# Performance work log

Measured on AMD Instinct MI355X. Metric: run time of the kernel, lower is better.

Reference implementation:

```python
import jax, jax.numpy as jnp
import numpy as np

B, D, N, C = 8192, 128, 64, 256

def setup_inputs() -> dict:
    key = jax.random.key(0)
    ks = jax.random.split(key, 7)
    s1 = 1.0 / np.sqrt(D)
    s2 = 1.0 / np.sqrt(C)
    return {
        "X": jax.random.normal(ks[0], (B, D, N), dtype=jnp.float32),
        "W1": jax.random.normal(ks[1], (D, C), dtype=jnp.float32) * s1,
        "b1": jax.random.normal(ks[2], (C,), dtype=jnp.float32) * s1,
        "W2": jax.random.normal(ks[3], (C, C), dtype=jnp.float32) * s2,
        "b2": jax.random.normal(ks[4], (C,), dtype=jnp.float32) * s2,
        "W3": jax.random.normal(ks[5], (C, 1), dtype=jnp.float32) * s2,
        "b3": jax.random.normal(ks[6], (1,), dtype=jnp.float32) * s2,
    }

def reference(X, W1, b1, W2, b2, W3, b3):
    # X: (B, D, N); each per-node slice X[:, :, i] goes through the shared MLP.
    # Batched over nodes: one GEMM instead of N tiny launches.
    h = jax.nn.relu(jnp.einsum('bdn,dc->bnc', X, W1) + b1)   # (B, N, C)
    h = jax.nn.relu(jnp.einsum('bnc,ce->bne', h, W2) + b2)   # (B, N, C)
    logits = jnp.einsum('bnc,co->bno', h, W3) + b3           # (B, N, 1)
    logits = logits[..., 0]                                   # (B, N)
    zeros = jnp.zeros((X.shape[0], 1), dtype=logits.dtype)    # add_zero=True
    return jnp.concatenate([zeros, logits], axis=1)           # (B, N+1)
```

## Files before the change

### kernel.cpp

```cpp
#include <hip/hip_runtime.h>
#include <hip/hip_bf16.h>

typedef unsigned short u16;
typedef unsigned int   u32;
typedef __attribute__((ext_vector_type(8))) short bf16x8;
typedef __attribute__((ext_vector_type(4))) float f32x4;

#define NB 8192

__device__ __forceinline__ u32 pack2bf(float a, float b) {
    __hip_bfloat162 h = __float22bfloat162_rn(make_float2(a, b));
    return *reinterpret_cast<u32*>(&h);
}

__device__ __forceinline__ u16 f2bf(float x) {
    u32 u = __float_as_uint(x);
    u32 r = u + 0x7FFFu + ((u >> 16) & 1u);
    return (u16)(r >> 16);
}

__global__ __launch_bounds__(256) void prep_weights(
    const float* __restrict__ W1, const float* __restrict__ W2,
    u16* __restrict__ w1fr, u16* __restrict__ w2fr)
{
    int tid = blockIdx.x * 256 + threadIdx.x;
    if (tid < 32768) {
        const int f = tid >> 9, r = tid & 511, l = r >> 3, j = r & 7;
        const int wv = f >> 4, mt = (f >> 2) & 3, ks = f & 3;
        const int c = 64 * wv + 16 * mt + (l & 15);
        const int d = 32 * ks + 8 * (l >> 4) + j;
        w1fr[tid] = f2bf(W1[d * 256 + c]);
    } else {
        const int t2 = tid - 32768;
        if (t2 < 65536) {
            const int f = t2 >> 9, r = t2 & 511, l = r >> 3, j = r & 7;
            const int wv = f >> 5, et = (f >> 3) & 3, ks = f & 7;
            const int e = 64 * wv + 16 * et + (l & 15);
            const int c = 32 * ks + 8 * (l >> 4) + j;
            w2fr[t2] = f2bf(W2[c * 256 + e]);
        }
    }
}

__global__ __launch_bounds__(256, 4) void fused_mlp(
    const float* __restrict__ X,
    const float* __restrict__ b1, const float* __restrict__ b2,
    const float* __restrict__ W3, const float* __restrict__ b3,
    const u16* __restrict__ w1fr, const u16* __restrict__ w2fr,
    float* __restrict__ out)
{
    __shared__ u16 smem[64 * 256];
    u16* xt   = smem;
    u16* h1s  = smem;
    float* partl = (float*)smem;

    const int tid = threadIdx.x;
    const int w   = tid >> 6;
    const int l   = tid & 63;
    const int lc  = l & 15;
    const int lk  = l >> 4;
    const int b   = blockIdx.x;
    const float* Xb = X + (size_t)b * 8192;

    const u16* w1b = w1fr + w * 8192  + l * 8;
    const u16* w2b = w2fr + w * 16384 + l * 8;

    #pragma unroll
    for (int it = 0; it < 4; ++it) {
        const int dc = w + 4 * it, d0 = dc << 3;
        float v[8];
        #pragma unroll
        for (int j = 0; j < 8; ++j) v[j] = Xb[(d0 + j) * 64 + l];
        u32 pk[4];
        #pragma unroll
        for (int j = 0; j < 4; ++j) pk[j] = pack2bf(v[2 * j], v[2 * j + 1]);
        *(uint4*)(xt + l * 128 + ((dc ^ lc) << 3)) = make_uint4(pk[0], pk[1], pk[2], pk[3]);
    }

    bf16x8 afrN[4];
    #pragma unroll
    for (int mt = 0; mt < 4; ++mt)
        afrN[mt] = *(const bf16x8*)(w1b + mt * 2048);
    __syncthreads();

    f32x4 acc[4][4];
    #pragma unroll
    for (int mt = 0; mt < 4; ++mt)
        #pragma unroll
        for (int nt = 0; nt < 4; ++nt) acc[mt][nt] = (f32x4){0.f, 0.f, 0.f, 0.f};

    #pragma unroll
    for (int ks = 0; ks < 4; ++ks) {
        bf16x8 afr[4], bfr[4];
        #pragma unroll
        for (int mt = 0; mt < 4; ++mt) afr[mt] = afrN[mt];
        if (ks < 3) {
            #pragma unroll
            for (int mt = 0; mt < 4; ++mt)
                afrN[mt] = *(const bf16x8*)(w1b + (mt * 4 + ks + 1) * 512);
        }
        #pragma unroll
        for (int nt = 0; nt < 4; ++nt)
            bfr[nt] = *(const bf16x8*)(xt + (16 * nt + lc) * 128 + (((4 * ks + lk) ^ lc) << 3));
        #pragma unroll
        for (int mt = 0; mt < 4; ++mt)
            #pragma unroll
            for (int nt = 0; nt < 4; ++nt)
                acc[mt][nt] = __builtin_amdgcn_mfma_f32_16x16x32_bf16(afr[mt], bfr[nt], acc[mt][nt], 0, 0, 0);
    }
    __syncthreads();

    #pragma unroll
    for (int mt = 0; mt < 4; ++mt) {
        const int c0 = 64 * w + 16 * mt + 4 * lk;
        const float4 bv = *(const float4*)(b1 + c0);
        #pragma unroll
        for (int nt = 0; nt < 4; ++nt) {
            const int n = 16 * nt + lc;
            float x0 = fmaxf(acc[mt][nt][0] + bv.x, 0.f);
            float x1 = fmaxf(acc[mt][nt][1] + bv.y, 0.f);
            float x2 = fmaxf(acc[mt][nt][2] + bv.z, 0.f);
            float x3 = fmaxf(acc[mt][nt][3] + bv.w, 0.f);
            const int chunk = (c0 >> 3) ^ lc;
            *(uint2*)(h1s + n * 256 + (chunk << 3) + (c0 & 7)) =
                make_uint2(pack2bf(x0, x1), pack2bf(x2, x3));
        }
    }

    bf16x8 bfrN[4];
    #pragma unroll
    for (int nt = 0; nt < 4; ++nt)
        bfrN[nt] = *(const bf16x8*)(w2b + nt * 4096);
    __syncthreads();

    f32x4 acc2[4][4];
    #pragma unroll
    for (int mt = 0; mt < 4; ++mt)
        #pragma unroll
        for (int nt = 0; nt < 4; ++nt) acc2[mt][nt] = (f32x4){0.f, 0.f, 0.f, 0.f};

    #pragma unroll
    for (int ks = 0; ks < 8; ++ks) {
        bf16x8 afr[4], bfr[4];
        #pragma unroll
        for (int nt = 0; nt < 4; ++nt) bfr[nt] = bfrN[nt];
        if (ks < 7) {
            #pragma unroll
            for (int nt = 0; nt < 4; ++nt)
                bfrN[nt] = *(const bf16x8*)(w2b + (nt * 8 + ks + 1) * 512);
        }
        #pragma unroll
        for (int mt = 0; mt < 4; ++mt)
            afr[mt] = *(const bf16x8*)(h1s + (16 * mt + lc) * 256 + (((4 * ks + lk) ^ lc) << 3));
        #pragma unroll
        for (int mt = 0; mt < 4; ++mt)
            #pragma unroll
            for (int nt = 0; nt < 4; ++nt)
                acc2[mt][nt] = __builtin_amdgcn_mfma_f32_16x16x32_bf16(afr[mt], bfr[nt], acc2[mt][nt], 0, 0, 0);
    }
    __syncthreads();

    float b2v[4], w3v[4];
    #pragma unroll
    for (int nt = 0; nt < 4; ++nt) {
        const int e = 64 * w + 16 * nt + lc;
        b2v[nt] = b2[e];
        w3v[nt] = W3[e];
    }
    #pragma unroll
    for (int mt = 0; mt < 4; ++mt) {
        #pragma unroll
        for (int j = 0; j < 4; ++j) {
            float s = 0.f;
            #pragma unroll
            for (int nt = 0; nt < 4; ++nt)
                s += fmaxf(acc2[mt][nt][j] + b2v[nt], 0.f) * w3v[nt];
            s += __shfl_xor(s, 1);
            s += __shfl_xor(s, 2);
            s += __shfl_xor(s, 4);
            s += __shfl_xor(s, 8);
            if (lc == 0) partl[w * 64 + 16 * mt + 4 * lk + j] = s;
        }
    }
    __syncthreads();

    if (tid < 64) {
        float s = partl[0 * 64 + tid] + partl[1 * 64 + tid] + partl[2 * 64 + tid] + partl[3 * 64 + tid] + b3[0];
        out[(size_t)b * 65 + 1 + tid] = s;
    } else if (tid == 64) {
        out[(size_t)b * 65] = 0.f;
    }
}

extern "C" void kernel_launch(void* const* d_in, const int* in_sizes, int n_in,
                              void* d_out, int out_size, void* d_ws, size_t ws_size,
                              hipStream_t stream) {
    const float* X  = (const float*)d_in[0];
    const float* W1 = (const float*)d_in[1];
    const float* b1 = (const float*)d_in[2];
    const float* W2 = (const float*)d_in[3];
    const float* b2 = (const float*)d_in[4];
    const float* W3 = (const float*)d_in[5];
    const float* b3 = (const float*)d_in[6];
    float* out = (float*)d_out;

    u16* w1fr = (u16*)d_ws;
    u16* w2fr = w1fr + 32768;

    prep_weights<<<384, 256, 0, stream>>>(W1, W2, w1fr, w2fr);
    fused_mlp<<<NB, 256, 0, stream>>>(X, b1, b2, W3, b3, w1fr, w2fr, out);
}
```

Baseline: 122.2 us.

## Split fused MLP across eight waves per block with separate LDS buffers

Doubles the block to 512 threads so each of eight waves owns 32 output channels instead of 64, halving per-wave accumulator registers and weight fragments, and re-lays out the prepped weight fragments to match. Gives X tile, hidden activations and partial sums their own shared buffers instead of aliasing one, which removes two block barriers. Folds the biases into the accumulator initialisation. The cost is more LDS per block (which may limit blocks per CU), and each wave now rereads the full activation tile from LDS for half the output work.

```diff
diff --git a/kernel.cpp b/kernel.cpp
--- a/kernel.cpp
+++ b/kernel.cpp
@@ -26,48 +26,47 @@
     int tid = blockIdx.x * 256 + threadIdx.x;
     if (tid < 32768) {
         const int f = tid >> 9, r = tid & 511, l = r >> 3, j = r & 7;
-        const int wv = f >> 4, mt = (f >> 2) & 3, ks = f & 3;
-        const int c = 64 * wv + 16 * mt + (l & 15);
+        const int p = f >> 3, mt = (f >> 2) & 1, ks = f & 3;
+        const int c = 32 * p + 16 * mt + (l & 15);
         const int d = 32 * ks + 8 * (l >> 4) + j;
         w1fr[tid] = f2bf(W1[d * 256 + c]);
     } else {
         const int t2 = tid - 32768;
         if (t2 < 65536) {
             const int f = t2 >> 9, r = t2 & 511, l = r >> 3, j = r & 7;
-            const int wv = f >> 5, et = (f >> 3) & 3, ks = f & 7;
-            const int e = 64 * wv + 16 * et + (l & 15);
-            const int c = 32 * ks + 8 * (l >> 4) + j;
-            w2fr[t2] = f2bf(W2[c * 256 + e]);
-        }
-    }
-}
-
-__global__ __launch_bounds__(256, 4) void fused_mlp(
+            const int q = f >> 4, et = (f >> 3) & 1, ks = f & 7;
+            const int e = 32 * q + 16 * et + (l & 15);
+            const int cc = 32 * ks + 8 * (l >> 4) + j;
+            w2fr[t2] = f2bf(W2[cc * 256 + e]);
+        }
+    }
+}
+
+__global__ __launch_bounds__(512, 6) void fused_mlp(
     const float* __restrict__ X,
     const float* __restrict__ b1, const float* __restrict__ b2,
     const float* __restrict__ W3, const float* __restrict__ b3,
     const u16* __restrict__ w1fr, const u16* __restrict__ w2fr,
     float* __restrict__ out)
 {
-    __shared__ u16 smem[64 * 256];
-    u16* xt   = smem;
-    u16* h1s  = smem;
-    float* partl = (float*)smem;
+    __shared__ __align__(16) u16 xt[64 * 128];
+    __shared__ __align__(16) u16 h1s[64 * 256];
+    __shared__ float partl[8][64];
 
     const int tid = threadIdx.x;
-    const int w   = tid >> 6;
+    const int wv  = tid >> 6;
     const int l   = tid & 63;
     const int lc  = l & 15;
     const int lk  = l >> 4;
     const int b   = blockIdx.x;
     const float* Xb = X + (size_t)b * 8192;
 
-    const u16* w1b = w1fr + w * 8192  + l * 8;
-    const u16* w2b = w2fr + w * 16384 + l * 8;
-
-    #pragma unroll
-    for (int it = 0; it < 4; ++it) {
-        const int dc = w + 4 * it, d0 = dc << 3;
+    const u16* w1b = w1fr + wv * 4096 + l * 8;
+    const u16* w2b = w2fr + wv * 8192 + l * 8;
+
+    #pragma unroll
+    for (int c2 = 0; c2 < 2; ++c2) {
+        const int dc = wv + 8 * c2, d0 = dc << 3;
         float v[8];
         #pragma unroll
         for (int j = 0; j < 8; ++j) v[j] = Xb[(d0 + j) * 64 + l];
@@ -77,77 +76,84 @@
         *(uint4*)(xt + l * 128 + ((dc ^ lc) << 3)) = make_uint4(pk[0], pk[1], pk[2], pk[3]);
     }
 
-    bf16x8 afrN[4];
-    #pragma unroll
-    for (int mt = 0; mt < 4; ++mt)
+    bf16x8 afrN[2];
+    #pragma unroll
+    for (int mt = 0; mt < 2; ++mt)
         afrN[mt] = *(const bf16x8*)(w1b + mt * 2048);
     __syncthreads();
 
-    f32x4 acc[4][4];
-    #pragma unroll
-    for (int mt = 0; mt < 4; ++mt)
-        #pragma unroll
-        for (int nt = 0; nt < 4; ++nt) acc[mt][nt] = (f32x4){0.f, 0.f, 0.f, 0.f};
+    f32x4 acc[2][4];
+    #pragma unroll
+    for (int mt = 0; mt < 2; ++mt) {
+        const float4 bq = *(const float4*)(b1 + 32 * wv + 16 * mt + 4 * lk);
+        #pragma unroll
+        for (int nt = 0; nt < 4; ++nt)
+            acc[mt][nt] = (f32x4){bq.x, bq.y, bq.z, bq.w};
+    }
 
     #pragma unroll
     for (int ks = 0; ks < 4; ++ks) {
-        bf16x8 afr[4], bfr[4];
-        #pragma unroll
-        for (int mt = 0; mt < 4; ++mt) afr[mt] = afrN[mt];
+        bf16x8 afr[2], bfr[4];
+        #pragma unroll
+        for (int mt = 0; mt < 2; ++mt) afr[mt] = afrN[mt];
         if (ks < 3) {
             #pragma unroll
-            for (int mt = 0; mt < 4; ++mt)
+            for (int mt = 0; mt < 2; ++mt)
                 afrN[mt] = *(const bf16x8*)(w1b + (mt * 4 + ks + 1) * 512);
         }
         #pragma unroll
         for (int nt = 0; nt < 4; ++nt)
             bfr[nt] = *(const bf16x8*)(xt + (16 * nt + lc) * 128 + (((4 * ks + lk) ^ lc) << 3));
         #pragma unroll
-        for (int mt = 0; mt < 4; ++mt)
+        for (int mt = 0; mt < 2; ++mt)
             #pragma unroll
             for (int nt = 0; nt < 4; ++nt)
                 acc[mt][nt] = __builtin_amdgcn_mfma_f32_16x16x32_bf16(afr[mt], bfr[nt], acc[mt][nt], 0, 0, 0);
     }
-    __syncthreads();
-
-    #pragma unroll
-    for (int mt = 0; mt < 4; ++mt) {
-        const int c0 = 64 * w + 16 * mt + 4 * lk;
-        const float4 bv = *(const float4*)(b1 + c0);
+
+    #pragma unroll
+    for (int mt = 0; mt < 2; ++mt) {
+        const int c0 = 32 * wv + 16 * mt + 4 * lk;
         #pragma unroll
         for (int nt = 0; nt < 4; ++nt) {
             const int n = 16 * nt + lc;
-            float x0 = fmaxf(acc[mt][nt][0] + bv.x, 0.f);
-            float x1 = fmaxf(acc[mt][nt][1] + bv.y, 0.f);
-            float x2 = fmaxf(acc[mt][nt][2] + bv.z, 0.f);
-            float x3 = fmaxf(acc[mt][nt][3] + bv.w, 0.f);
+            float x0 = fmaxf(acc[mt][nt][0], 0.f);
+            float x1 = fmaxf(acc[mt][nt][1], 0.f);
+            float x2 = fmaxf(acc[mt][nt][2], 0.f);
+            float x3 = fmaxf(acc[mt][nt][3], 0.f);
             const int chunk = (c0 >> 3) ^ lc;
             *(uint2*)(h1s + n * 256 + (chunk << 3) + (c0 & 7)) =
                 make_uint2(pack2bf(x0, x1), pack2bf(x2, x3));
         }
     }
 
-    bf16x8 bfrN[4];
-    #pragma unroll
-    for (int nt = 0; nt < 4; ++nt)
-        bfrN[nt] = *(const bf16x8*)(w2b + nt * 4096);
+    bf16x8 bfrN[2];
+    #pragma unroll
+    for (int et = 0; et < 2; ++et)
+        bfrN[et] = *(const bf16x8*)(w2b + et * 4096);
     __syncthreads();
 
-    f32x4 acc2[4][4];
-    #pragma unroll
-    for (int mt = 0; mt < 4; ++mt)
-        #pragma unroll
-        for (int nt = 0; nt < 4; ++nt) acc2[mt][nt] = (f32x4){0.f, 0.f, 0.f, 0.f};
+    f32x4 acc2[4][2];
+    float w3v[2];
+    #pragma unroll
+    for (int et = 0; et < 2; ++et) {
+        const int e = 32 * wv + 16 * et + lc;
+        const float bv = b2[e];
+        w3v[et] = W3[e];
+        #pragma unroll
+        for (int mt = 0; mt < 4; ++mt)
+            acc2[mt][et] = (f32x4){bv, bv, bv, bv};
+    }
 
     #pragma unroll
     for (int ks = 0; ks < 8; ++ks) {
-        bf16x8 afr[4], bfr[4];
-        #pragma unroll
-        for (int nt = 0; nt < 4; ++nt) bfr[nt] = bfrN[nt];
+        bf16x8 afr[4], bfr[2];
+        #pragma unroll
+        for (int et = 0; et < 2; ++et) bfr[et] = bfrN[et];
         if (ks < 7) {
             #pragma unroll
-            for (int nt = 0; nt < 4; ++nt)
-                bfrN[nt] = *(const bf16x8*)(w2b + (nt * 8 + ks + 1) * 512);
+            for (int et = 0; et < 2; ++et)
+                bfrN[et] = *(const bf16x8*)(w2b + (et * 8 + ks + 1) * 512);
         }
         #pragma unroll
         for (int mt = 0; mt < 4; ++mt)
@@ -155,37 +161,29 @@
         #pragma unroll
         for (int mt = 0; mt < 4; ++mt)
             #pragma unroll
-            for (int nt = 0; nt < 4; ++nt)
-                acc2[mt][nt] = __builtin_amdgcn_mfma_f32_16x16x32_bf16(afr[mt], bfr[nt], acc2[mt][nt], 0, 0, 0);
-    }
-    __syncthreads();
-
-    float b2v[4], w3v[4];
-    #pragma unroll
-    for (int nt = 0; nt < 4; ++nt) {
-        const int e = 64 * w + 16 * nt + lc;
-        b2v[nt] = b2[e];
-        w3v[nt] = W3[e];
-    }
+            for (int et = 0; et < 2; ++et)
+                acc2[mt][et] = __builtin_amdgcn_mfma_f32_16x16x32_bf16(afr[mt], bfr[et], acc2[mt][et], 0, 0, 0);
+    }
+
     #pragma unroll
     for (int mt = 0; mt < 4; ++mt) {
         #pragma unroll
         for (int j = 0; j < 4; ++j) {
-            float s = 0.f;
-            #pragma unroll
-            for (int nt = 0; nt < 4; ++nt)
-                s += fmaxf(acc2[mt][nt][j] + b2v[nt], 0.f) * w3v[nt];
+            float s = fmaxf(acc2[mt][0][j], 0.f) * w3v[0]
+                    + fmaxf(acc2[mt][1][j], 0.f) * w3v[1];
             s += __shfl_xor(s, 1);
             s += __shfl_xor(s, 2);
             s += __shfl_xor(s, 4);
             s += __shfl_xor(s, 8);
-            if (lc == 0) partl[w * 64 + 16 * mt + 4 * lk + j] = s;
+            if (lc == 0) partl[wv][16 * mt + 4 * lk + j] = s;
         }
     }
     __syncthreads();
 
     if (tid < 64) {
-        float s = partl[0 * 64 + tid] + partl[1 * 64 + tid] + partl[2 * 64 + tid] + partl[3 * 64 + tid] + b3[0];
+        float s = b3[0];
+        #pragma unroll
+        for (int k = 0; k < 8; ++k) s += partl[k][tid];
         out[(size_t)b * 65 + 1 + tid] = s;
     } else if (tid == 64) {
         out[(size_t)b * 65] = 0.f;
@@ -207,6 +205,8 @@
     u16* w1fr = (u16*)d_ws;
     u16* w2fr = w1fr + 32768;
 
+    const int B = in_sizes[0] / (128 * 64);
+
     prep_weights<<<384, 256, 0, stream>>>(W1, W2, w1fr, w2fr);
-    fused_mlp<<<NB, 256, 0, stream>>>(X, b1, b2, W3, b3, w1fr, w2fr, out);
-}
+    fused_mlp<<<B, 512, 0, stream>>>(X, b1, b2, W3, b3, w1fr, w2fr, out);
+}
```

New measurement: 140.7 us. 15.2% more time.
